# Optimization experiments

Measured on AMD Instinct MI355X. Metric: run time of the kernel, lower is better.

The kernel has to match this reference:

```python
import jax, jax.numpy as jnp
import numpy as np

GMIN, GMAX = 0.1, 1.0
DIMS = [3, 256, 256, 256, 1]

def setup_inputs() -> dict:
    key = jax.random.key(0)
    ks = jax.random.split(key, 12)
    inp = {"pos": jax.random.normal(ks[0], (1048576, 3), dtype=jnp.float32)}
    for i in range(4):
        fan_in = DIMS[i]
        bound = 1.0 / np.sqrt(fan_in)
        inp[f"W{i}"] = jax.random.uniform(ks[1 + 2 * i], (fan_in, DIMS[i + 1]), jnp.float32, -bound, bound)
        inp[f"b{i}"] = jax.random.uniform(ks[2 + 2 * i], (DIMS[i + 1],), jnp.float32, -bound, bound)
    for i in range(3):
        inp[f"sigma{i}"] = jax.random.uniform(ks[9 + i], (256,), jnp.float32, GMIN, GMAX)
    return inp

def _gauss(x, sigma):
    # Gaussian activation: exp(-x^2 / (2*sigma^2)), sigma learnable per-feature
    return jnp.exp(-jnp.square(x) / (2.0 * jnp.square(sigma)))

def _softplus8(x):
    # torch Softplus(beta=1, threshold=8): linear beyond threshold
    return jnp.where(x > 8.0, x, jnp.log1p(jnp.exp(jnp.minimum(x, 8.0))))

def reference(pos, W0, b0, W1, b1, W2, b2, W3, b3, sigma0, sigma1, sigma2):
    h = _gauss(pos @ W0 + b0, sigma0)      # [N,256]
    h = _gauss(h @ W1 + b1, sigma1)        # [N,256]
    h = _gauss(h @ W2 + b2, sigma2)        # [N,256]
    return _softplus8(h @ W3 + b3)         # [N,1]
```

## Files before the change

kernel.cpp:

```cpp
#include <hip/hip_runtime.h>
#include <hip/hip_bf16.h>

typedef __attribute__((ext_vector_type(8))) short short8;
typedef __attribute__((ext_vector_type(4))) float f32x4;
typedef __attribute__((ext_vector_type(2))) unsigned int uint2v;

#define LOG2E 1.4426950408889634f
#define LN2   0.6931471805599453f

__device__ __forceinline__ unsigned short f2bf(float f) {
    union { float f; unsigned u; } v; v.f = f;
    unsigned u = v.u;
    u += 0x7fffu + ((u >> 16) & 1u);
    return (unsigned short)(u >> 16);
}
__device__ __forceinline__ float bf2f(unsigned short h) {
    union { unsigned u; float f; } v; v.u = ((unsigned)h) << 16;
    return v.f;
}
__device__ __forceinline__ unsigned pk_bf16(float a, float b) {
    __hip_bfloat162 t = __float22bfloat162_rn(float2{a, b});
    union { __hip_bfloat162 b; unsigned u; } v; v.b = t;
    return v.u;
}

__global__ void pack_kernel(const float* __restrict__ W0, const float* __restrict__ W1,
                            const float* __restrict__ W2,
                            const float* __restrict__ s0, const float* __restrict__ s1,
                            const float* __restrict__ s2,
                            unsigned short* __restrict__ wp, float* __restrict__ negc) {
    int tid = blockIdx.x * 256 + threadIdx.x;
    if (tid < 8192) {
        int j = tid & 7, lane = (tid >> 3) & 63, t = tid >> 9;
        int k = ((lane >> 4) * 8) + j;
        int n = ((t >> 3) * 128) + (((t >> 2) & 1) * 64) + 4 * (lane & 15) + (t & 3);
        unsigned short v = 0;
        if (k < 9) {
            int d = k / 3, m = k - d * 3;
            float w = W0[d * 256 + n];
            unsigned short wh = f2bf(w);
            v = (m == 1) ? f2bf(w - bf2f(wh)) : wh;
        }
        wp[tid] = v;
    } else if (tid < 139264) {
        int e = tid - 8192;
        const float* W = W1;
        if (e >= 65536) { W = W2; e -= 65536; }
        int j = e & 7, lane = (e >> 3) & 63, ks = (e >> 9) & 7, t = e >> 12;
        int k = ks * 32 + ((lane >> 4) * 8) + j;
        int n = ((t >> 3) * 128) + (((t >> 2) & 1) * 64) + 4 * (lane & 15) + (t & 3);
        wp[tid] = f2bf(W[k * 256 + n]);
    }
    if (tid < 768) {
        const float* s = (tid < 256) ? s0 : (tid < 512 ? s1 : s2);
        float sv = s[tid & 255];
        negc[tid] = -LOG2E / (2.0f * sv * sv);
    }
}

constexpr int ROWS = 64;
constexpr int HSTR = 264;
constexpr int ASTR = 40;

template <int NKS, int SSTR>
__device__ __forceinline__ void layer(const unsigned short* __restrict__ src,
                                      const unsigned short* __restrict__ wpk,
                                      const float* __restrict__ bias,
                                      const float* __restrict__ ncp,
                                      unsigned short* __restrict__ hdst,
                                      int rgrp, int chalf, int i16, int q, bool presync) {
    f32x4 acc[2][8];
#pragma unroll
    for (int rg = 0; rg < 2; ++rg)
#pragma unroll
        for (int nt = 0; nt < 8; ++nt)
            acc[rg][nt] = f32x4{0.f, 0.f, 0.f, 0.f};

    const int lane = q * 16 + i16;
    const short8* wp8 = (const short8*)wpk + (chalf * 8 * NKS) * 64 + lane;
    const unsigned short* abase = src + (rgrp * 32 + i16) * SSTR + q * 8;
#pragma unroll
    for (int ks = 0; ks < NKS; ++ks) {
        short8 a0 = *(const short8*)(abase + ks * 32);
        short8 a1 = *(const short8*)(abase + 16 * SSTR + ks * 32);
#pragma unroll
        for (int s = 0; s < 8; ++s) {
            short8 wf = wp8[(s * NKS + ks) * 64];
            acc[0][s] = __builtin_amdgcn_mfma_f32_16x16x32_bf16(a0, wf, acc[0][s], 0, 0, 0);
            acc[1][s] = __builtin_amdgcn_mfma_f32_16x16x32_bf16(a1, wf, acc[1][s], 0, 0, 0);
        }
    }
    if (presync) __syncthreads();

#pragma unroll
    for (int p = 0; p < 2; ++p) {
        const int ce = chalf * 128 + p * 64 + 4 * i16;
        const f32x4 bb = *(const f32x4*)(bias + ce);
        const f32x4 np = *(const f32x4*)(ncp + ce);
#pragma unroll
        for (int rg = 0; rg < 2; ++rg) {
            int rbase = rgrp * 32 + rg * 16 + q * 4;
#pragma unroll
            for (int rr = 0; rr < 4; ++rr) {
                float x0 = acc[rg][4*p+0][rr] + bb[0];
                float x1 = acc[rg][4*p+1][rr] + bb[1];
                float x2 = acc[rg][4*p+2][rr] + bb[2];
                float x3 = acc[rg][4*p+3][rr] + bb[3];
                float g0 = __builtin_amdgcn_exp2f(x0 * x0 * np[0]);
                float g1 = __builtin_amdgcn_exp2f(x1 * x1 * np[1]);
                float g2 = __builtin_amdgcn_exp2f(x2 * x2 * np[2]);
                float g3 = __builtin_amdgcn_exp2f(x3 * x3 * np[3]);
                uint2v v;
                v[0] = pk_bf16(g0, g1);
                v[1] = pk_bf16(g2, g3);
                *(uint2v*)&hdst[(rbase + rr) * HSTR + ce] = v;
            }
        }
    }
    __syncthreads();
}

__global__ __launch_bounds__(256, 4) void mlp_kernel(
    const float* __restrict__ pos,
    const float* __restrict__ b0, const float* __restrict__ b1,
    const float* __restrict__ b2,
    const float* __restrict__ W3, const float* __restrict__ b3,
    const unsigned short* __restrict__ Wp,
    const float* __restrict__ negc,
    float* __restrict__ out)
{
    __shared__ unsigned short h[ROWS * HSTR];
    __shared__ unsigned short A0[ROWS * ASTR];

    const int tid  = threadIdx.x;
    const int lane = tid & 63;
    const int wave = tid >> 6;
    const int rgrp = wave >> 1, chalf = wave & 1;
    const int i16  = lane & 15, q = lane >> 4;
    const long row0 = (long)blockIdx.x * ROWS;

    if (tid < ROWS) {
        const float* pp = pos + (row0 + tid) * 3;
        float p0 = pp[0], p1 = pp[1], p2 = pp[2];
        short h0 = (short)f2bf(p0); short l0 = (short)f2bf(p0 - bf2f((unsigned short)h0));
        short h1 = (short)f2bf(p1); short l1 = (short)f2bf(p1 - bf2f((unsigned short)h1));
        short h2 = (short)f2bf(p2); short l2 = (short)f2bf(p2 - bf2f((unsigned short)h2));
        unsigned short* arow = A0 + tid * ASTR;
        *(short8*)(arow + 0)  = short8{h0, h0, l0, h1, h1, l1, h2, h2};
        *(short8*)(arow + 8)  = short8{l2, 0, 0, 0, 0, 0, 0, 0};
        *(short8*)(arow + 16) = short8{0, 0, 0, 0, 0, 0, 0, 0};
        *(short8*)(arow + 24) = short8{0, 0, 0, 0, 0, 0, 0, 0};
    }
    __syncthreads();

    layer<1, ASTR>(A0, Wp, b0, negc, h, rgrp, chalf, i16, q, false);
    layer<8, HSTR>(h, Wp + 8192, b1, negc + 256, h, rgrp, chalf, i16, q, true);
    layer<8, HSTR>(h, Wp + 73728, b2, negc + 512, h, rgrp, chalf, i16, q, true);

    {
        int r = tid >> 2, qq = tid & 3;
        const unsigned short* hrow = h + r * HSTR;
        float s = 0.0f;
#pragma unroll
        for (int i = 0; i < 8; ++i) {
            int c = (qq + 4 * i) * 8;
            short8 hv = *(const short8*)(hrow + c);
            f32x4 wA = *(const f32x4*)(W3 + c);
            f32x4 wB = *(const f32x4*)(W3 + c + 4);
#pragma unroll
            for (int jj = 0; jj < 4; ++jj) {
                s = fmaf(bf2f((unsigned short)hv[jj]), wA[jj], s);
                s = fmaf(bf2f((unsigned short)hv[4 + jj]), wB[jj], s);
            }
        }
        s += __shfl_xor(s, 1);
        s += __shfl_xor(s, 2);
        if (qq == 0) {
            float x  = s + b3[0];
            float xm = fminf(x, 8.0f);
            float e  = __builtin_amdgcn_exp2f(xm * LOG2E);
            float sp = __builtin_amdgcn_logf(1.0f + e) * LN2;
            out[row0 + r] = (x > 8.0f) ? x : sp;
        }
    }
}

extern "C" void kernel_launch(void* const* d_in, const int* in_sizes, int n_in,
                              void* d_out, int out_size, void* d_ws, size_t ws_size,
                              hipStream_t stream) {
    const float* pos = (const float*)d_in[0];
    const float* W0  = (const float*)d_in[1];
    const float* b0  = (const float*)d_in[2];
    const float* W1  = (const float*)d_in[3];
    const float* b1  = (const float*)d_in[4];
    const float* W2  = (const float*)d_in[5];
    const float* b2  = (const float*)d_in[6];
    const float* W3  = (const float*)d_in[7];
    const float* b3  = (const float*)d_in[8];
    const float* s0  = (const float*)d_in[9];
    const float* s1  = (const float*)d_in[10];
    const float* s2  = (const float*)d_in[11];

    unsigned short* wp = (unsigned short*)d_ws;
    float* negc = (float*)((char*)d_ws + 278528);

    pack_kernel<<<544, 256, 0, stream>>>(W0, W1, W2, s0, s1, s2, wp, negc);

    int nrows = in_sizes[0] / 3;
    int nblk  = nrows / ROWS;
    mlp_kernel<<<nblk, 256, 0, stream>>>(pos, b0, b1, b2, W3, b3, wp, negc,
                                         (float*)d_out);
}
```

Measured before the change: 459.8 us.

## Software-pipeline weight and activation loads and move epilogue before barrier

The MFMA loop now double-buffers weight fragments in register groups of four and prefetches the next k-step's activation fragments, so global and LDS loads overlap with matrix instructions. The bias, Gaussian and bf16 packing epilogue is computed into registers before the write-after-read barrier, leaving only the LDS stores after it and letting slower waves do useful work while they wait. The higher register use is covered by relaxing launch bounds from 4 to 3 blocks per SM, which trades occupancy for latency hiding.

Measured after the change: 455.6 us. Within noise of the previous version (-0.9%).

```diff
diff --git a/kernel.cpp b/kernel.cpp
--- a/kernel.cpp
+++ b/kernel.cpp
@@ -79,27 +79,49 @@
     const int lane = q * 16 + i16;
     const short8* wp8 = (const short8*)wpk + (chalf * 8 * NKS) * 64 + lane;
     const unsigned short* abase = src + (rgrp * 32 + i16) * SSTR + q * 8;
+
+    short8 wcur[4], wnxt[4];
+    short8 a0 = *(const short8*)(abase);
+    short8 a1 = *(const short8*)(abase + 16 * SSTR);
+    short8 na0 = a0, na1 = a1;
+#pragma unroll
+    for (int s = 0; s < 4; ++s) wcur[s] = wp8[(s * NKS) * 64];
+
 #pragma unroll
     for (int ks = 0; ks < NKS; ++ks) {
-        short8 a0 = *(const short8*)(abase + ks * 32);
-        short8 a1 = *(const short8*)(abase + 16 * SSTR + ks * 32);
-#pragma unroll
-        for (int s = 0; s < 8; ++s) {
-            short8 wf = wp8[(s * NKS + ks) * 64];
-            acc[0][s] = __builtin_amdgcn_mfma_f32_16x16x32_bf16(a0, wf, acc[0][s], 0, 0, 0);
-            acc[1][s] = __builtin_amdgcn_mfma_f32_16x16x32_bf16(a1, wf, acc[1][s], 0, 0, 0);
-        }
-    }
-    if (presync) __syncthreads();
-
+#pragma unroll
+        for (int g = 0; g < 2; ++g) {
+            if (g == 0) {
+#pragma unroll
+                for (int s = 0; s < 4; ++s)
+                    wnxt[s] = wp8[((4 + s) * NKS + ks) * 64];
+            } else if (ks + 1 < NKS) {
+#pragma unroll
+                for (int s = 0; s < 4; ++s)
+                    wnxt[s] = wp8[(s * NKS + ks + 1) * 64];
+                na0 = *(const short8*)(abase + (ks + 1) * 32);
+                na1 = *(const short8*)(abase + 16 * SSTR + (ks + 1) * 32);
+            }
+#pragma unroll
+            for (int s = 0; s < 4; ++s) {
+                int nt = g * 4 + s;
+                acc[0][nt] = __builtin_amdgcn_mfma_f32_16x16x32_bf16(a0, wcur[s], acc[0][nt], 0, 0, 0);
+                acc[1][nt] = __builtin_amdgcn_mfma_f32_16x16x32_bf16(a1, wcur[s], acc[1][nt], 0, 0, 0);
+            }
+#pragma unroll
+            for (int s = 0; s < 4; ++s) wcur[s] = wnxt[s];
+            if (g == 1) { a0 = na0; a1 = na1; }
+        }
+    }
+
+    uint2v av[2][2][4];
 #pragma unroll
     for (int p = 0; p < 2; ++p) {
         const int ce = chalf * 128 + p * 64 + 4 * i16;
         const f32x4 bb = *(const f32x4*)(bias + ce);
         const f32x4 np = *(const f32x4*)(ncp + ce);
 #pragma unroll
-        for (int rg = 0; rg < 2; ++rg) {
-            int rbase = rgrp * 32 + rg * 16 + q * 4;
+        for (int rg = 0; rg < 2; ++rg)
 #pragma unroll
             for (int rr = 0; rr < 4; ++rr) {
                 float x0 = acc[rg][4*p+0][rr] + bb[0];
@@ -113,14 +135,25 @@
                 uint2v v;
                 v[0] = pk_bf16(g0, g1);
                 v[1] = pk_bf16(g2, g3);
-                *(uint2v*)&hdst[(rbase + rr) * HSTR + ce] = v;
-            }
+                av[p][rg][rr] = v;
+            }
+    }
+    if (presync) __syncthreads();
+#pragma unroll
+    for (int p = 0; p < 2; ++p) {
+        const int ce = chalf * 128 + p * 64 + 4 * i16;
+#pragma unroll
+        for (int rg = 0; rg < 2; ++rg) {
+            int rbase = rgrp * 32 + rg * 16 + q * 4;
+#pragma unroll
+            for (int rr = 0; rr < 4; ++rr)
+                *(uint2v*)&hdst[(rbase + rr) * HSTR + ce] = av[p][rg][rr];
         }
     }
     __syncthreads();
 }
 
-__global__ __launch_bounds__(256, 4) void mlp_kernel(
+__global__ __launch_bounds__(256, 3) void mlp_kernel(
     const float* __restrict__ pos,
     const float* __restrict__ b0, const float* __restrict__ b1,
     const float* __restrict__ b2,
```

## Split waves by 64-column strips and compute activations before barrier

Applied to the files above, without the earlier changes.

Changes the wave work split from a 2x2 grid of 32 rows by 128 columns to each wave owning all 64 rows and one 64-column strip. Each wave now loads each weight fragment once and reuses it across four row groups, and the packed weight layout is reordered to match. The Gaussian activation is computed into registers before the pre-store barrier, so only the LDS stores wait on the other waves. The risks are more LDS A-fragment reads per wave, higher register pressure from holding the packed outputs, and lower occupancy from the launch bound dropping from 4 to 3.

Measured after the change: 398.2 us. -13.4%, faster.

```diff
diff --git a/kernel.cpp b/kernel.cpp
--- a/kernel.cpp
+++ b/kernel.cpp
@@ -31,24 +31,24 @@
                             unsigned short* __restrict__ wp, float* __restrict__ negc) {
     int tid = blockIdx.x * 256 + threadIdx.x;
     if (tid < 8192) {
-        int j = tid & 7, lane = (tid >> 3) & 63, t = tid >> 9;
+        int j = tid & 7, lane = (tid >> 3) & 63, ct = (tid >> 9) & 3, w = tid >> 11;
         int k = ((lane >> 4) * 8) + j;
-        int n = ((t >> 3) * 128) + (((t >> 2) & 1) * 64) + 4 * (lane & 15) + (t & 3);
+        int n = w * 64 + 4 * (lane & 15) + ct;
         unsigned short v = 0;
         if (k < 9) {
             int d = k / 3, m = k - d * 3;
-            float w = W0[d * 256 + n];
-            unsigned short wh = f2bf(w);
-            v = (m == 1) ? f2bf(w - bf2f(wh)) : wh;
+            float wv = W0[d * 256 + n];
+            unsigned short wh = f2bf(wv);
+            v = (m == 1) ? f2bf(wv - bf2f(wh)) : wh;
         }
         wp[tid] = v;
     } else if (tid < 139264) {
         int e = tid - 8192;
         const float* W = W1;
         if (e >= 65536) { W = W2; e -= 65536; }
-        int j = e & 7, lane = (e >> 3) & 63, ks = (e >> 9) & 7, t = e >> 12;
+        int j = e & 7, lane = (e >> 3) & 63, ct = (e >> 9) & 3, ks = (e >> 11) & 7, w = e >> 14;
         int k = ks * 32 + ((lane >> 4) * 8) + j;
-        int n = ((t >> 3) * 128) + (((t >> 2) & 1) * 64) + 4 * (lane & 15) + (t & 3);
+        int n = w * 64 + 4 * (lane & 15) + ct;
         wp[tid] = f2bf(W[k * 256 + n]);
     }
     if (tid < 768) {
@@ -68,59 +68,66 @@
                                       const float* __restrict__ bias,
                                       const float* __restrict__ ncp,
                                       unsigned short* __restrict__ hdst,
-                                      int rgrp, int chalf, int i16, int q, bool presync) {
-    f32x4 acc[2][8];
-#pragma unroll
-    for (int rg = 0; rg < 2; ++rg)
-#pragma unroll
-        for (int nt = 0; nt < 8; ++nt)
-            acc[rg][nt] = f32x4{0.f, 0.f, 0.f, 0.f};
+                                      int w, int i16, int q, bool presync) {
+    f32x4 acc[4][4];
+#pragma unroll
+    for (int rg = 0; rg < 4; ++rg)
+#pragma unroll
+        for (int ct = 0; ct < 4; ++ct)
+            acc[rg][ct] = f32x4{0.f, 0.f, 0.f, 0.f};
 
     const int lane = q * 16 + i16;
-    const short8* wp8 = (const short8*)wpk + (chalf * 8 * NKS) * 64 + lane;
-    const unsigned short* abase = src + (rgrp * 32 + i16) * SSTR + q * 8;
+    const short8* wp8 = (const short8*)wpk + (w * NKS * 4) * 64 + lane;
+    const unsigned short* abase = src + i16 * SSTR + q * 8;
+
 #pragma unroll
     for (int ks = 0; ks < NKS; ++ks) {
-        short8 a0 = *(const short8*)(abase + ks * 32);
-        short8 a1 = *(const short8*)(abase + 16 * SSTR + ks * 32);
-#pragma unroll
-        for (int s = 0; s < 8; ++s) {
-            short8 wf = wp8[(s * NKS + ks) * 64];
-            acc[0][s] = __builtin_amdgcn_mfma_f32_16x16x32_bf16(a0, wf, acc[0][s], 0, 0, 0);
-            acc[1][s] = __builtin_amdgcn_mfma_f32_16x16x32_bf16(a1, wf, acc[1][s], 0, 0, 0);
-        }
-    }
+        short8 a[4];
+#pragma unroll
+        for (int rg = 0; rg < 4; ++rg)
+            a[rg] = *(const short8*)(abase + rg * 16 * SSTR + ks * 32);
+#pragma unroll
+        for (int ct = 0; ct < 4; ++ct) {
+            short8 wf = wp8[(ks * 4 + ct) * 64];
+#pragma unroll
+            for (int rg = 0; rg < 4; ++rg)
+                acc[rg][ct] = __builtin_amdgcn_mfma_f32_16x16x32_bf16(a[rg], wf, acc[rg][ct], 0, 0, 0);
+        }
+    }
+
+    const int ce = w * 64 + 4 * i16;
+    const f32x4 bb = *(const f32x4*)(bias + ce);
+    const f32x4 np = *(const f32x4*)(ncp + ce);
+    uint2v av[4][4];
+#pragma unroll
+    for (int rg = 0; rg < 4; ++rg)
+#pragma unroll
+        for (int rr = 0; rr < 4; ++rr) {
+            float x0 = acc[rg][0][rr] + bb[0];
+            float x1 = acc[rg][1][rr] + bb[1];
+            float x2 = acc[rg][2][rr] + bb[2];
+            float x3 = acc[rg][3][rr] + bb[3];
+            float g0 = __builtin_amdgcn_exp2f(x0 * x0 * np[0]);
+            float g1 = __builtin_amdgcn_exp2f(x1 * x1 * np[1]);
+            float g2 = __builtin_amdgcn_exp2f(x2 * x2 * np[2]);
+            float g3 = __builtin_amdgcn_exp2f(x3 * x3 * np[3]);
+            uint2v v;
+            v[0] = pk_bf16(g0, g1);
+            v[1] = pk_bf16(g2, g3);
+            av[rg][rr] = v;
+        }
     if (presync) __syncthreads();
-
-#pragma unroll
-    for (int p = 0; p < 2; ++p) {
-        const int ce = chalf * 128 + p * 64 + 4 * i16;
-        const f32x4 bb = *(const f32x4*)(bias + ce);
-        const f32x4 np = *(const f32x4*)(ncp + ce);
-#pragma unroll
-        for (int rg = 0; rg < 2; ++rg) {
-            int rbase = rgrp * 32 + rg * 16 + q * 4;
-#pragma unroll
-            for (int rr = 0; rr < 4; ++rr) {
-                float x0 = acc[rg][4*p+0][rr] + bb[0];
-                float x1 = acc[rg][4*p+1][rr] + bb[1];
-                float x2 = acc[rg][4*p+2][rr] + bb[2];
-                float x3 = acc[rg][4*p+3][rr] + bb[3];
-                float g0 = __builtin_amdgcn_exp2f(x0 * x0 * np[0]);
-                float g1 = __builtin_amdgcn_exp2f(x1 * x1 * np[1]);
-                float g2 = __builtin_amdgcn_exp2f(x2 * x2 * np[2]);
-                float g3 = __builtin_amdgcn_exp2f(x3 * x3 * np[3]);
-                uint2v v;
-                v[0] = pk_bf16(g0, g1);
-                v[1] = pk_bf16(g2, g3);
-                *(uint2v*)&hdst[(rbase + rr) * HSTR + ce] = v;
-            }
-        }
+#pragma unroll
+    for (int rg = 0; rg < 4; ++rg) {
+        int rbase = rg * 16 + q * 4;
+#pragma unroll
+        for (int rr = 0; rr < 4; ++rr)
+            *(uint2v*)&hdst[(rbase + rr) * HSTR + ce] = av[rg][rr];
     }
     __syncthreads();
 }
 
-__global__ __launch_bounds__(256, 4) void mlp_kernel(
+__global__ __launch_bounds__(256, 3) void mlp_kernel(
     const float* __restrict__ pos,
     const float* __restrict__ b0, const float* __restrict__ b1,
     const float* __restrict__ b2,
@@ -135,7 +142,6 @@
     const int tid  = threadIdx.x;
     const int lane = tid & 63;
     const int wave = tid >> 6;
-    const int rgrp = wave >> 1, chalf = wave & 1;
     const int i16  = lane & 15, q = lane >> 4;
     const long row0 = (long)blockIdx.x * ROWS;
 
@@ -153,9 +159,9 @@
     }
     __syncthreads();
 
-    layer<1, ASTR>(A0, Wp, b0, negc, h, rgrp, chalf, i16, q, false);
-    layer<8, HSTR>(h, Wp + 8192, b1, negc + 256, h, rgrp, chalf, i16, q, true);
-    layer<8, HSTR>(h, Wp + 73728, b2, negc + 512, h, rgrp, chalf, i16, q, true);
+    layer<1, ASTR>(A0, Wp, b0, negc, h, wave, i16, q, false);
+    layer<8, HSTR>(h, Wp + 8192, b1, negc + 256, h, wave, i16, q, true);
+    layer<8, HSTR>(h, Wp + 73728, b2, negc + 512, h, wave, i16, q, true);
 
     {
         int r = tid >> 2, qq = tid & 3;
```
